# Optimization experiments

Measured on AMD Instinct MI355X. Metric: run time of the kernel, lower is better.

## Reference

```python
import jax, jax.numpy as jnp
import numpy as np


def _apply_1q_batched(state, gate, q):
    # state: (B,2,2,2,2) complex; gate: (B,2,2) complex; acts on qubit q
    state = jnp.moveaxis(state, q + 1, -1)
    state = jnp.einsum('bij,b...j->b...i', gate, state)
    return jnp.moveaxis(state, -1, q + 1)


def _apply_cnot(state, c, t):
    # flip target bit where control bit == 1
    s0, s1 = jnp.split(state, 2, axis=c + 1)
    s1 = jnp.flip(s1, axis=t + 1)
    return jnp.concatenate([s0, s1], axis=c + 1)


def _quantum_features(angles, params):
    # angles: (B,4) RY rotation angles; params: (4,) RZ angles
    B = angles.shape[0]
    state = jnp.zeros((B, 16), jnp.complex64).at[:, 0].set(1.0).reshape(B, 2, 2, 2, 2)
    # RY(x_i) on each wire (batched angle per sample)
    for q in range(4):
        th = 0.5 * angles[:, q]
        c, s = jnp.cos(th), jnp.sin(th)
        gate = jnp.stack([jnp.stack([c, -s], -1), jnp.stack([s, c], -1)], -2).astype(jnp.complex64)
        state = _apply_1q_batched(state, gate, q)
    # RZ(params[i]) on wire i followed by CNOT(i, (i+1)%4), interleaved as in source
    pc = params.astype(jnp.complex64)
    for q in range(4):
        ph = jnp.exp(jnp.array([-0.5j, 0.5j], jnp.complex64) * pc[q])
        shp = [1, 1, 1, 1, 1]
        shp[q + 1] = 2
        state = state * ph.reshape(shp)
        state = _apply_cnot(state, q, (q + 1) % 4)
    probs = state.real ** 2 + state.imag ** 2  # (B,2,2,2,2)
    feats = []
    for q in range(4):
        axes = tuple(a for a in range(1, 5) if a != q + 1)
        p = probs.sum(axes)  # (B,2)
        feats.append(p[:, 0] - p[:, 1])  # <Z_q>
    return jnp.stack(feats, -1)  # (B,4)


def _deconv2x2(x, w, b):
    # PyTorch ConvTranspose2d with kernel=stride=2, padding=0 (non-overlapping)
    # x: (B,Ci,H,W), w: (Ci,Co,2,2), b: (Co,)
    B, Ci, H, W = x.shape
    Co = w.shape[1]
    y = jnp.einsum('bchw,codk->bohdwk', x, w).reshape(B, Co, 2 * H, 2 * W)
    return y + b[None, :, None, None]


def setup_inputs() -> dict:
    key = jax.random.key(0)
    ks = jax.random.split(key, 10)
    B = 16384
    return {
        'x': jax.random.uniform(ks[0], (B, 1, 28, 28), jnp.float32),
        'var_params': jax.random.normal(ks[1], (4,), jnp.float32),
        'w_lat': jax.random.normal(ks[2], (224, 4), jnp.float32) * 0.3,
        'b_lat': jax.random.normal(ks[3], (224,), jnp.float32) * 0.05,
        'w_fc': jax.random.normal(ks[4], (392, 224), jnp.float32) * 0.05,
        'b_fc': jax.random.normal(ks[5], (392,), jnp.float32) * 0.05,
        'w_d1': jax.random.normal(ks[6], (8, 4, 2, 2), jnp.float32) * 0.2,
        'b_d1': jax.random.normal(ks[7], (4,), jnp.float32) * 0.05,
        'w_d2': jax.random.normal(ks[8], (4, 1, 2, 2), jnp.float32) * 0.2,
        'b_d2': jax.random.normal(ks[9], (1,), jnp.float32) * 0.05,
    }


def reference(x, var_params, w_lat, b_lat, w_fc, b_fc, w_d1, b_d1, w_d2, b_d2):
    # quadrant means -> 4 angles per sample
    quad = jnp.stack([
        x[:, 0, :14, :14].mean((1, 2)),
        x[:, 0, :14, 14:].mean((1, 2)),
        x[:, 0, 14:, :14].mean((1, 2)),
        x[:, 0, 14:, 14:].mean((1, 2)),
    ], axis=1)  # (B,4)
    qf = _quantum_features(quad, var_params)  # (B,4)
    latent = jax.nn.relu(qf @ w_lat.T + b_lat)  # (B,224)
    h = jax.nn.relu(latent @ w_fc.T + b_fc)  # (B,392)
    h = h.reshape(-1, 8, 7, 7)
    h = jax.nn.relu(_deconv2x2(h, w_d1, b_d1))  # (B,4,14,14)
    out = jax.nn.sigmoid(_deconv2x2(h, w_d2, b_d2))  # (B,1,28,28)
    return out
```

## Files before the change

kernel.cpp:

```cpp
#include <hip/hip_runtime.h>
#include <math.h>

#define G 16
#define HS2 400
#define LSTR 232

typedef __attribute__((ext_vector_type(8))) __bf16 bf16x8;
typedef __attribute__((ext_vector_type(4))) float f32x4;
typedef __attribute__((ext_vector_type(2))) float f32x2;

__global__ void wconv_kernel(const float* __restrict__ w_fc, __bf16* __restrict__ wb) {
  int tile = blockIdx.x;
  int kt   = blockIdx.y;
  int lane = threadIdx.x;
  int n  = tile * 16 + (lane & 15);
  int k0 = kt * 32 + (lane >> 4) * 8;
  bf16x8 v;
  if (n < 392) {
    const float* src = w_fc + (size_t)n * 224 + k0;
    float4 f0 = *(const float4*)(src);
    float4 f1 = *(const float4*)(src + 4);
    v[0] = (__bf16)f0.x; v[1] = (__bf16)f0.y; v[2] = (__bf16)f0.z; v[3] = (__bf16)f0.w;
    v[4] = (__bf16)f1.x; v[5] = (__bf16)f1.y; v[6] = (__bf16)f1.z; v[7] = (__bf16)f1.w;
  } else {
    #pragma unroll
    for (int j = 0; j < 8; ++j) v[j] = (__bf16)0.f;
  }
  *(bf16x8*)(wb + ((size_t)(tile * 7 + kt) * 64 + lane) * 8) = v;
}

__global__ __launch_bounds__(256, 6) void fused_kernel(
    const float* __restrict__ x, const float* __restrict__ params,
    const __bf16* __restrict__ wb,
    const float* __restrict__ w_lat, const float* __restrict__ b_lat,
    const float* __restrict__ b_fc,
    const float* __restrict__ w_d1, const float* __restrict__ b_d1,
    const float* __restrict__ w_d2, const float* __restrict__ b_d2,
    float* __restrict__ out, int B)
{
  __shared__ __align__(16) __bf16 latb[G * LSTR];
  __shared__ __align__(16) __bf16 hbuf[G * HS2];
  __shared__ __align__(16) float qfs[G * 4];
  __shared__ float wd1[128];
  __shared__ float wd2[16];
  __shared__ float bd1[4];
  const int t = threadIdx.x;
  const int wv = t >> 6;
  const int lane = t & 63;
  const int s0g = blockIdx.x * G;
  if (s0g >= B) return;

  if (t < 128) wd1[t] = w_d1[t];
  else if (t < 144) wd2[t - 128] = w_d2[t - 128];
  else if (t < 148) bd1[t - 144] = b_d1[t - 144];

  {
    const float* xb = x + (size_t)(s0g + wv * 4) * 784;
    float acc[4][4];
    #pragma unroll
    for (int i = 0; i < 4; ++i)
      #pragma unroll
      for (int q = 0; q < 4; ++q) acc[i][q] = 0.f;
    for (int i4 = lane; i4 < 196; i4 += 64) {
      int base = i4 * 4;
      int r = base / 28;
      int cb = base - r * 28;
      float bt = (r >= 14) ? 1.f : 0.f;
      float tp = 1.f - bt;
      float w0[4], w1[4], w2[4], w3[4];
      #pragma unroll
      for (int e = 0; e < 4; ++e) {
        float lf = ((cb + e) < 14) ? 1.f : 0.f;
        float rf = 1.f - lf;
        w0[e] = tp * lf; w1[e] = tp * rf; w2[e] = bt * lf; w3[e] = bt * rf;
      }
      #pragma unroll
      for (int smp = 0; smp < 4; ++smp) {
        f32x4 v = __builtin_nontemporal_load((const f32x4*)(xb + smp * 784 + base));
        #pragma unroll
        for (int e = 0; e < 4; ++e) {
          acc[smp][0] = fmaf(v[e], w0[e], acc[smp][0]);
          acc[smp][1] = fmaf(v[e], w1[e], acc[smp][1]);
          acc[smp][2] = fmaf(v[e], w2[e], acc[smp][2]);
          acc[smp][3] = fmaf(v[e], w3[e], acc[smp][3]);
        }
      }
    }
    #pragma unroll
    for (int smp = 0; smp < 4; ++smp)
      #pragma unroll
      for (int q = 0; q < 4; ++q)
        #pragma unroll
        for (int o = 32; o > 0; o >>= 1)
          acc[smp][q] += __shfl_down(acc[smp][q], o, 64);
    if (lane == 0) {
      const float inv = 1.f / 196.f;
      #pragma unroll
      for (int smp = 0; smp < 4; ++smp) {
        float4 o;
        o.x = acc[smp][0] * inv; o.y = acc[smp][1] * inv;
        o.z = acc[smp][2] * inv; o.w = acc[smp][3] * inv;
        *(float4*)(qfs + (wv * 4 + smp) * 4) = o;
      }
    }
  }

  {
    const int sub = lane >> 4;
    const int i   = lane & 15;
    const int s   = wv * 4 + sub;
    float4 mn = *(const float4*)(qfs + s * 4);
    float c_[4], s_[4];
    c_[0] = __cosf(0.5f * mn.x); s_[0] = __sinf(0.5f * mn.x);
    c_[1] = __cosf(0.5f * mn.y); s_[1] = __sinf(0.5f * mn.y);
    c_[2] = __cosf(0.5f * mn.z); s_[2] = __sinf(0.5f * mn.z);
    c_[3] = __cosf(0.5f * mn.w); s_[3] = __sinf(0.5f * mn.w);
    float re = (((i >> 3) & 1) ? s_[0] : c_[0]) * (((i >> 2) & 1) ? s_[1] : c_[1])
             * (((i >> 1) & 1) ? s_[2] : c_[2]) * ((i & 1) ? s_[3] : c_[3]);
    float im = 0.f;
    #pragma unroll
    for (int q = 0; q < 4; ++q) {
      float hp = 0.5f * params[q];
      float sp = __sinf(hp), cp = __cosf(hp);
      int qb = 3 - q;
      float sg = ((i >> qb) & 1) ? sp : -sp;
      float r0 = re, i0 = im;
      re = r0 * cp - i0 * sg;
      im = r0 * sg + i0 * cp;
      int cm = 1 << qb;
      int tm = 1 << (3 - ((q + 1) & 3));
      int srcI = (i & cm) ? (i ^ tm) : i;
      int srcLane = (lane & ~15) | srcI;
      re = __shfl(re, srcLane, 64);
      im = __shfl(im, srcLane, 64);
    }
    float p = re * re + im * im;
    float z[4];
    #pragma unroll
    for (int q = 0; q < 4; ++q) {
      int qb = 3 - q;
      float v = ((i >> qb) & 1) ? -p : p;
      v += __shfl_xor(v, 1, 16);
      v += __shfl_xor(v, 2, 16);
      v += __shfl_xor(v, 4, 16);
      v += __shfl_xor(v, 8, 16);
      z[q] = v;
    }
    if (i < 4) {
      float zv = (i == 0) ? z[0] : (i == 1) ? z[1] : (i == 2) ? z[2] : z[3];
      qfs[s * 4 + i] = zv;
    }
  }

  #pragma unroll
  for (int sl = 0; sl < 4; ++sl) {
    int s = wv * 4 + sl;
    float4 q4 = *(const float4*)(qfs + s * 4);
    for (int j = lane; j < 224; j += 64) {
      float4 w = *(const float4*)(w_lat + j * 4);
      float a = b_lat[j];
      a = fmaf(q4.x, w.x, a);
      a = fmaf(q4.y, w.y, a);
      a = fmaf(q4.z, w.z, a);
      a = fmaf(q4.w, w.w, a);
      latb[s * LSTR + j] = (__bf16)fmaxf(a, 0.f);
    }
  }
  __syncthreads();

  {
    const int m = lane & 15;
    const int kq = lane >> 4;
    const __bf16* arow = latb + m * LSTR + kq * 8;
    for (int tile = wv; tile < 25; tile += 4) {
      f32x4 acc = {0.f, 0.f, 0.f, 0.f};
      const bf16x8* bp = (const bf16x8*)(wb + ((size_t)(tile * 7) * 64 + lane) * 8);
      #pragma unroll
      for (int kt = 0; kt < 7; ++kt) {
        bf16x8 a = *(const bf16x8*)(arow + kt * 32);
        bf16x8 b = bp[kt * 64];
        acc = __builtin_amdgcn_mfma_f32_16x16x32_bf16(a, b, acc, 0, 0, 0);
      }
      int j = tile * 16 + m;
      if (j < 392) {
        float bf = b_fc[j];
        #pragma unroll
        for (int r = 0; r < 4; ++r)
          hbuf[(kq * 4 + r) * HS2 + j] = (__bf16)fmaxf(acc[r] + bf, 0.f);
      }
    }
  }
  __syncthreads();

  const float bd2v = b_d2[0];
  for (int v = t; v < G * 196; v += 256) {
    int s = v / 196;
    int p = v - s * 196;
    int Y = p / 14;
    int X = p - Y * 14;
    int y = Y >> 1, ey = Y & 1, xx = X >> 1, ex = X & 1;
    const __bf16* hs = hbuf + s * HS2 + y * 7 + xx;
    float hv[8];
    #pragma unroll
    for (int ci = 0; ci < 8; ++ci) hv[ci] = (float)hs[ci * 49];
    float o1[4];
    #pragma unroll
    for (int co = 0; co < 4; ++co) {
      float a = bd1[co];
      #pragma unroll
      for (int ci = 0; ci < 8; ++ci)
        a = fmaf(hv[ci], wd1[ci * 16 + co * 4 + ey * 2 + ex], a);
      o1[co] = fmaxf(a, 0.f);
    }
    size_t basep = (size_t)(s0g + s) * 784;
    #pragma unroll
    for (int dy = 0; dy < 2; ++dy) {
      float v0 = bd2v, v1 = bd2v;
      #pragma unroll
      for (int co = 0; co < 4; ++co) {
        v0 = fmaf(o1[co], wd2[co * 4 + dy * 2 + 0], v0);
        v1 = fmaf(o1[co], wd2[co * 4 + dy * 2 + 1], v1);
      }
      f32x2 o;
      o[0] = 1.f / (1.f + __expf(-v0));
      o[1] = 1.f / (1.f + __expf(-v1));
      __builtin_nontemporal_store(o, (f32x2*)(out + basep + (size_t)(2 * Y + dy) * 28 + 2 * X));
    }
  }
}

extern "C" void kernel_launch(void* const* d_in, const int* in_sizes, int n_in,
                              void* d_out, int out_size, void* d_ws, size_t ws_size,
                              hipStream_t stream) {
  const float* x          = (const float*)d_in[0];
  const float* var_params = (const float*)d_in[1];
  const float* w_lat      = (const float*)d_in[2];
  const float* b_lat      = (const float*)d_in[3];
  const float* w_fc       = (const float*)d_in[4];
  const float* b_fc       = (const float*)d_in[5];
  const float* w_d1       = (const float*)d_in[6];
  const float* b_d1       = (const float*)d_in[7];
  const float* w_d2       = (const float*)d_in[8];
  const float* b_d2       = (const float*)d_in[9];
  float* out = (float*)d_out;

  __bf16* wb = (__bf16*)d_ws;

  int B = in_sizes[0] / 784;
  wconv_kernel<<<dim3(25, 7), 64, 0, stream>>>(w_fc, wb);
  fused_kernel<<<(B + G - 1) / G, 256, 0, stream>>>(
      x, var_params, wb, w_lat, b_lat, b_fc, w_d1, b_d1, w_d2, b_d2, out, B);
}
```

Baseline: 145.0 us.

## Double block size to 512 threads, batch x loads, store hidden in fp32

The fused kernel now launches 512 threads per block, so each wave handles 2 samples instead of 4 in the quadrant-mean and latent stages, and the MFMA tile loop is spread over 8 waves. All x loads for a wave are issued up front into registers before the reduction, giving more memory-level parallelism. The hidden buffer switches from bf16 to fp32 with stride 396, removing conversions and possibly reducing LDS bank conflicts, at the cost of more shared memory per block. The quantum stage now has half its lanes doing redundant work, and the larger LDS footprint may limit how many blocks fit on a CU.

```diff
diff --git a/kernel.cpp b/kernel.cpp
--- a/kernel.cpp
+++ b/kernel.cpp
@@ -2,7 +2,7 @@
 #include <math.h>
 
 #define G 16
-#define HS2 400
+#define HS 396
 #define LSTR 232
 
 typedef __attribute__((ext_vector_type(8))) __bf16 bf16x8;
@@ -29,7 +29,7 @@
   *(bf16x8*)(wb + ((size_t)(tile * 7 + kt) * 64 + lane) * 8) = v;
 }
 
-__global__ __launch_bounds__(256, 6) void fused_kernel(
+__global__ __launch_bounds__(512, 8) void fused_kernel(
     const float* __restrict__ x, const float* __restrict__ params,
     const __bf16* __restrict__ wb,
     const float* __restrict__ w_lat, const float* __restrict__ b_lat,
@@ -39,7 +39,7 @@
     float* __restrict__ out, int B)
 {
   __shared__ __align__(16) __bf16 latb[G * LSTR];
-  __shared__ __align__(16) __bf16 hbuf[G * HS2];
+  __shared__ __align__(16) float hbuf[G * HS];
   __shared__ __align__(16) float qfs[G * 4];
   __shared__ float wd1[128];
   __shared__ float wd2[16];
@@ -55,13 +55,26 @@
   else if (t < 148) bd1[t - 144] = b_d1[t - 144];
 
   {
-    const float* xb = x + (size_t)(s0g + wv * 4) * 784;
-    float acc[4][4];
-    #pragma unroll
-    for (int i = 0; i < 4; ++i)
+    const float* xb = x + (size_t)(s0g + wv * 2) * 784;
+    f32x4 vb[2][4];
+    #pragma unroll
+    for (int smp = 0; smp < 2; ++smp)
+      #pragma unroll
+      for (int it = 0; it < 4; ++it) {
+        int i4 = lane + it * 64;
+        if (i4 < 196)
+          vb[smp][it] = __builtin_nontemporal_load((const f32x4*)(xb + smp * 784 + i4 * 4));
+        else
+          vb[smp][it] = (f32x4){0.f, 0.f, 0.f, 0.f};
+      }
+    float acc[2][4];
+    #pragma unroll
+    for (int i = 0; i < 2; ++i)
       #pragma unroll
       for (int q = 0; q < 4; ++q) acc[i][q] = 0.f;
-    for (int i4 = lane; i4 < 196; i4 += 64) {
+    #pragma unroll
+    for (int it = 0; it < 4; ++it) {
+      int i4 = lane + it * 64;
       int base = i4 * 4;
       int r = base / 28;
       int cb = base - r * 28;
@@ -75,8 +88,8 @@
         w0[e] = tp * lf; w1[e] = tp * rf; w2[e] = bt * lf; w3[e] = bt * rf;
       }
       #pragma unroll
-      for (int smp = 0; smp < 4; ++smp) {
-        f32x4 v = __builtin_nontemporal_load((const f32x4*)(xb + smp * 784 + base));
+      for (int smp = 0; smp < 2; ++smp) {
+        f32x4 v = vb[smp][it];
         #pragma unroll
         for (int e = 0; e < 4; ++e) {
           acc[smp][0] = fmaf(v[e], w0[e], acc[smp][0]);
@@ -87,7 +100,7 @@
       }
     }
     #pragma unroll
-    for (int smp = 0; smp < 4; ++smp)
+    for (int smp = 0; smp < 2; ++smp)
       #pragma unroll
       for (int q = 0; q < 4; ++q)
         #pragma unroll
@@ -96,11 +109,11 @@
     if (lane == 0) {
       const float inv = 1.f / 196.f;
       #pragma unroll
-      for (int smp = 0; smp < 4; ++smp) {
+      for (int smp = 0; smp < 2; ++smp) {
         float4 o;
         o.x = acc[smp][0] * inv; o.y = acc[smp][1] * inv;
         o.z = acc[smp][2] * inv; o.w = acc[smp][3] * inv;
-        *(float4*)(qfs + (wv * 4 + smp) * 4) = o;
+        *(float4*)(qfs + (wv * 2 + smp) * 4) = o;
       }
     }
   }
@@ -108,7 +121,7 @@
   {
     const int sub = lane >> 4;
     const int i   = lane & 15;
-    const int s   = wv * 4 + sub;
+    const int s   = wv * 2 + (sub & 1);
     float4 mn = *(const float4*)(qfs + s * 4);
     float c_[4], s_[4];
     c_[0] = __cosf(0.5f * mn.x); s_[0] = __sinf(0.5f * mn.x);
@@ -146,15 +159,15 @@
       v += __shfl_xor(v, 8, 16);
       z[q] = v;
     }
-    if (i < 4) {
+    if (sub < 2 && i < 4) {
       float zv = (i == 0) ? z[0] : (i == 1) ? z[1] : (i == 2) ? z[2] : z[3];
       qfs[s * 4 + i] = zv;
     }
   }
 
   #pragma unroll
-  for (int sl = 0; sl < 4; ++sl) {
-    int s = wv * 4 + sl;
+  for (int sl = 0; sl < 2; ++sl) {
+    int s = wv * 2 + sl;
     float4 q4 = *(const float4*)(qfs + s * 4);
     for (int j = lane; j < 224; j += 64) {
       float4 w = *(const float4*)(w_lat + j * 4);
@@ -172,7 +185,7 @@
     const int m = lane & 15;
     const int kq = lane >> 4;
     const __bf16* arow = latb + m * LSTR + kq * 8;
-    for (int tile = wv; tile < 25; tile += 4) {
+    for (int tile = wv; tile < 25; tile += 8) {
       f32x4 acc = {0.f, 0.f, 0.f, 0.f};
       const bf16x8* bp = (const bf16x8*)(wb + ((size_t)(tile * 7) * 64 + lane) * 8);
       #pragma unroll
@@ -186,23 +199,23 @@
         float bf = b_fc[j];
         #pragma unroll
         for (int r = 0; r < 4; ++r)
-          hbuf[(kq * 4 + r) * HS2 + j] = (__bf16)fmaxf(acc[r] + bf, 0.f);
+          hbuf[(kq * 4 + r) * HS + j] = fmaxf(acc[r] + bf, 0.f);
       }
     }
   }
   __syncthreads();
 
   const float bd2v = b_d2[0];
-  for (int v = t; v < G * 196; v += 256) {
+  for (int v = t; v < G * 196; v += 512) {
     int s = v / 196;
     int p = v - s * 196;
     int Y = p / 14;
     int X = p - Y * 14;
     int y = Y >> 1, ey = Y & 1, xx = X >> 1, ex = X & 1;
-    const __bf16* hs = hbuf + s * HS2 + y * 7 + xx;
+    const float* hs = hbuf + s * HS + y * 7 + xx;
     float hv[8];
     #pragma unroll
-    for (int ci = 0; ci < 8; ++ci) hv[ci] = (float)hs[ci * 49];
+    for (int ci = 0; ci < 8; ++ci) hv[ci] = hs[ci * 49];
     float o1[4];
     #pragma unroll
     for (int co = 0; co < 4; ++co) {
@@ -248,6 +261,6 @@
 
   int B = in_sizes[0] / 784;
   wconv_kernel<<<dim3(25, 7), 64, 0, stream>>>(w_fc, wb);
-  fused_kernel<<<(B + G - 1) / G, 256, 0, stream>>>(
+  fused_kernel<<<(B + G - 1) / G, 512, 0, stream>>>(
       x, var_params, wb, w_lat, b_lat, b_fc, w_d1, b_d1, w_d2, b_d2, out, B);
 }
```

After: 137.4 us. 1.06x faster.
